# Kernel optimization log

Hardware: AMD Instinct MI355X
Metric: run time of the kernel (lower is better)

Reference implementation:

```python
import jax, jax.numpy as jnp
import numpy as np

VOCAB = 512
EMB = 256
HID = 64
T_HORIZON = 0.05


def setup_inputs() -> dict:
    key = jax.random.key(0)
    ks = jax.random.split(key, 6)
    B, L = 32, 4096
    x = jax.random.randint(ks[0], (B, L), 0, VOCAB, dtype=jnp.int64 if jax.config.jax_enable_x64 else jnp.int32)
    emb_table = jax.random.normal(ks[1], (VOCAB, EMB), dtype=jnp.float32)
    W1 = jax.random.normal(ks[2], (EMB, HID), dtype=jnp.float32) * (1.0 / np.sqrt(EMB))
    b1 = jnp.zeros((HID,), dtype=jnp.float32)
    W2 = jax.random.normal(ks[3], (HID, VOCAB), dtype=jnp.float32) * (1.0 / np.sqrt(HID))
    b2 = jnp.full((VOCAB,), 0.1, dtype=jnp.float32)  # torch: bias.data.fill_(0.1)
    return {"x": x, "emb_table": emb_table, "W1": W1, "b1": b1, "W2": W2, "b2": b2, "steps": 5}


def reference(x, emb_table, W1, b1, W2, b2, steps):
    """Vectorized Gillespie-style Markov jump simulation.

    Equivalent to the torch loop: intensity is computed once per step from the
    current state, then every (b, l) position samples a candidate next state
    from softmax(intensity) with the self-transition zeroed and renormalized
    (== categorical over logits with the current state masked to -inf), and
    accepts it with prob 1 - exp(-rate * dt).
    """
    V = emb_table.shape[0]
    dt = T_HORIZON / steps
    key = jax.random.key(42)
    keys = jax.random.split(key, steps)
    vocab_ids = jnp.arange(V)

    def step(x_t, k):
        # intensity: [B, L, V]
        h = jax.nn.relu(emb_table[x_t] @ W1 + b1)
        intensity = h @ W2 + b2
        # mask self-transition (softmax * (1 - onehot) then renormalize)
        self_mask = x_t[..., None] == vocab_ids  # [B, L, V] bool
        masked_logits = jnp.where(self_mask, -jnp.inf, intensity)
        k1, k2 = jax.random.split(k)
        next_state = jax.random.categorical(k1, masked_logits)  # [B, L]
        rate = jnp.take_along_axis(intensity, next_state[..., None], axis=-1)[..., 0]
        accept_prob = 1.0 - jnp.exp(-rate * dt)
        u = jax.random.uniform(k2, x_t.shape, dtype=rate.dtype)
        x_t = jnp.where(u < accept_prob, next_state.astype(x_t.dtype), x_t)
        return x_t, None

    x_final, _ = jax.lax.scan(step, x, keys)
    return x_final
```

## Files before the change

kernel.cpp:

```cpp
#include <hip/hip_runtime.h>
#include <stdint.h>


#define VOCAB 512
#define EMB   256
#define HID   64
#define NPOS  (32 * 4096)
#define STEPS 5
#define PPW   8
#define NWAVES (NPOS / PPW)

__host__ __device__ __forceinline__ void tf2x32(uint32_t k0, uint32_t k1,
                                                uint32_t x0, uint32_t x1,
                                                uint32_t& o0, uint32_t& o1) {
  uint32_t ks2 = k0 ^ k1 ^ 0x1BD11BDAu;
  x0 += k0; x1 += k1;
#define TFR(r) { x0 += x1; x1 = (x1 << (r)) | (x1 >> (32 - (r))); x1 ^= x0; }
  TFR(13) TFR(15) TFR(26) TFR(6)
  x0 += k1;  x1 += ks2 + 1u;
  TFR(17) TFR(29) TFR(16) TFR(24)
  x0 += ks2; x1 += k0 + 2u;
  TFR(13) TFR(15) TFR(26) TFR(6)
  x0 += k0;  x1 += k1 + 3u;
  TFR(17) TFR(29) TFR(16) TFR(24)
  x0 += k1;  x1 += ks2 + 4u;
  TFR(13) TFR(15) TFR(26) TFR(6)
  x0 += ks2; x1 += k0 + 5u;
#undef TFR
  o0 = x0; o1 = x1;
}

struct Keys {
  uint32_t k1a[STEPS], k1b[STEPS];
  uint32_t k2a[STEPS], k2b[STEPS];
};

__global__ __launch_bounds__(512)
void build_table(const float* __restrict__ emb,
                 const float* __restrict__ W1,
                 const float* __restrict__ b1,
                 const float* __restrict__ W2,
                 const float* __restrict__ b2,
                 float* __restrict__ I,
                 float* __restrict__ pthr) {
  const int s   = blockIdx.x;
  const int tid = threadIdx.x;
  __shared__ double part[8][HID];
  __shared__ double hd[HID];
  __shared__ float  redmax[8];

  const int hid = tid & (HID - 1);
  const int kq  = tid >> 6;
  const float* e = emb + s * EMB;
  double acc = 0.0;
#pragma unroll
  for (int k = kq; k < EMB; k += 8)
    acc += (double)e[k] * (double)W1[k * HID + hid];
  part[kq][hid] = acc;
  __syncthreads();
  if (kq == 0) {
    const double a = ((part[0][hid] + part[1][hid]) + (part[2][hid] + part[3][hid]))
                   + ((part[4][hid] + part[5][hid]) + (part[6][hid] + part[7][hid]));
    const float m = (float)a + b1[hid];
    hd[hid] = (double)(m > 0.0f ? m : 0.0f);
  }
  __syncthreads();

  double acc2 = 0.0;
#pragma unroll
  for (int k = 0; k < HID; ++k)
    acc2 += hd[k] * (double)W2[k * VOCAB + tid];
  const float val = (float)acc2 + b2[tid];
  I[s * VOCAB + tid] = val;

  float lmax = val;
  for (int off = 32; off > 0; off >>= 1)
    lmax = fmaxf(lmax, __shfl_xor(lmax, off, 64));
  if ((tid & 63) == 0) redmax[tid >> 6] = lmax;
  __syncthreads();
  if (tid == 0) {
    float m = redmax[0];
#pragma unroll
    for (int i = 1; i < 8; ++i) m = fmaxf(m, redmax[i]);
    const float z = (-m) * 0.01f;
    pthr[s] = 1.0f - (float)exp((double)z);
  }
}

__global__ __launch_bounds__(256)
void markov_kernel(const int* __restrict__ x_in,
                   const float* __restrict__ I,
                   const float* __restrict__ pthr,
                   int* __restrict__ x_out,
                   Keys K) {
  __shared__ float sp[VOCAB];
  sp[threadIdx.x]       = pthr[threadIdx.x];
  sp[threadIdx.x + 256] = pthr[threadIdx.x + 256];
  __syncthreads();

  const int gtid = blockIdx.x * blockDim.x + threadIdx.x;
  const int wave = gtid >> 6;
  const int lane = gtid & 63;
  const int base = wave * PPW;
  const float TINYF = 1.17549435e-38f;

  const int qp = lane / 5;
  const int qt = lane - qp * 5;
  float u40 = 0.0f;
  if (lane < PPW * STEPS) {
    uint32_t w0, w1;
    tf2x32(K.k2a[qt], K.k2b[qt], 0u, (uint32_t)(base + qp), w0, w1);
    u40 = __uint_as_float((((w0 ^ w1) >> 9) | 0x3f800000u)) - 1.0f;
  }
  int scur = (lane < PPW) ? x_in[base + lane] : 0;

  const int s_of_q = __shfl(scur, qp, 64);
  const bool cand = (lane < PPW * STEPS) && (u40 < sp[s_of_q]);
  unsigned long long mask = __ballot(cand);

  while (mask) {
    const int q = (int)__builtin_ctzll(mask);
    mask &= mask - 1;
    const int p = q / 5;
    const int t = q - p * 5;
    const int s = __builtin_amdgcn_readfirstlane(__shfl(scur, p, 64));

    const float* row = I + s * VOCAB;
    float best = -__builtin_inff();
    int bidx = 0;
    const uint32_t fbase = ((uint32_t)(base + p) << 9) + (uint32_t)lane;
#pragma unroll
    for (int j = 0; j < VOCAB / 64; ++j) {
      const int v = lane + (j << 6);
      uint32_t w0, w1;
      tf2x32(K.k1a[t], K.k1b[t], 0u, fbase + ((uint32_t)j << 6), w0, w1);
      const uint32_t bits = w0 ^ w1;
      float uf = __uint_as_float((bits >> 9) | 0x3f800000u) - 1.0f;
      if (uf == 0.0f) uf = TINYF;
      const float g = -logf(-logf(uf));
      if (v != s) {
        const float val = row[v] + g;
        if (val > best) { best = val; bidx = v; }
      }
    }
    for (int off = 32; off > 0; off >>= 1) {
      const float ob = __shfl_xor(best, off, 64);
      const int   oi = __shfl_xor(bidx, off, 64);
      if (ob > best || (ob == best && oi < bidx)) { best = ob; bidx = oi; }
    }
    bidx = __builtin_amdgcn_readfirstlane(bidx);
    const float rate = row[bidx];
    const float z = (-rate) * 0.01f;
    const float pacc = 1.0f - (float)exp((double)z);
    const float u = __shfl(u40, q, 64);
    if (u < pacc) {
      if (lane == p) scur = bidx;
      const unsigned long long fut =
          (((1ull << (p * 5 + 5)) - 1) & ~((1ull << (q + 1)) - 1));
      const float pnew = sp[bidx];
      const unsigned long long nb = __ballot(u40 < pnew) & fut;
      mask = (mask & ~fut) | nb;
    }
  }
  if (lane < PPW) x_out[base + lane] = scur;
}

extern "C" void kernel_launch(void* const* d_in, const int* in_sizes, int n_in,
                              void* d_out, int out_size, void* d_ws, size_t ws_size,
                              hipStream_t stream) {
  const int*   x   = (const int*)d_in[0];
  const float* emb = (const float*)d_in[1];
  const float* W1  = (const float*)d_in[2];
  const float* b1  = (const float*)d_in[3];
  const float* W2  = (const float*)d_in[4];
  const float* b2  = (const float*)d_in[5];
  float* I    = (float*)d_ws;
  float* pthr = (float*)d_ws + VOCAB * VOCAB;
  int* out = (int*)d_out;

  Keys K;
  for (int t = 0; t < STEPS; ++t) {
    uint32_t Sa, Sb;
    tf2x32(0u, 42u, 0u, (uint32_t)t, Sa, Sb);
    tf2x32(Sa, Sb, 0u, 0u, K.k1a[t], K.k1b[t]);
    tf2x32(Sa, Sb, 0u, 1u, K.k2a[t], K.k2b[t]);
  }

  build_table<<<VOCAB, 512, 0, stream>>>(emb, W1, b1, W2, b2, I, pthr);
  markov_kernel<<<(NWAVES * 64) / 256, 256, 0, stream>>>(x, I, pthr, out, K);
}
```

Measured before the change: 121.5 us.

## Drop shared threshold table, shrink blocks, hoist row loads ahead of RNG

The per-block shared-memory copy of the acceptance threshold table and its barrier are removed, and thresholds are now read directly from global memory. Blocks shrink to 128 threads with a min-blocks-per-CU launch bound. The 8 intensity-row loads are issued before the Threefry computations so their latency overlaps with the RNG ALU work. This trades barrier and LDS setup per block for scattered global reads and possible register pressure from the hoisted arrays.

After: 116.0 us. 4.5% less time.

```diff
diff --git a/kernel.cpp b/kernel.cpp
--- a/kernel.cpp
+++ b/kernel.cpp
@@ -2,13 +2,13 @@
 #include <stdint.h>
 
 
-#define VOCAB 512
-#define EMB   256
-#define HID   64
-#define NPOS  (32 * 4096)
-#define STEPS 5
-#define PPW   8
-#define NWAVES (NPOS / PPW)
+#define VOCAB  512
+#define EMB    256
+#define HID    64
+#define NPOS   (32 * 4096)
+#define STEPS  5
+#define PPW    8
+#define CHUNKS (NPOS / PPW)
 
 __host__ __device__ __forceinline__ void tf2x32(uint32_t k0, uint32_t k1,
                                                 uint32_t x0, uint32_t x1,
@@ -87,35 +87,30 @@
   }
 }
 
-__global__ __launch_bounds__(256)
+__global__ __launch_bounds__(128, 4)
 void markov_kernel(const int* __restrict__ x_in,
                    const float* __restrict__ I,
                    const float* __restrict__ pthr,
                    int* __restrict__ x_out,
                    Keys K) {
-  __shared__ float sp[VOCAB];
-  sp[threadIdx.x]       = pthr[threadIdx.x];
-  sp[threadIdx.x + 256] = pthr[threadIdx.x + 256];
-  __syncthreads();
-
-  const int gtid = blockIdx.x * blockDim.x + threadIdx.x;
-  const int wave = gtid >> 6;
-  const int lane = gtid & 63;
-  const int base = wave * PPW;
+  const int lane  = threadIdx.x & 63;
+  const int chunk = (blockIdx.x << 1) | (threadIdx.x >> 6);
+  const int base  = chunk * PPW;
+  const int qp = lane / 5;
+  const int qt = lane - qp * 5;
   const float TINYF = 1.17549435e-38f;
 
-  const int qp = lane / 5;
-  const int qt = lane - qp * 5;
+  int scur = (lane < PPW) ? x_in[base + lane] : 0;
+
   float u40 = 0.0f;
   if (lane < PPW * STEPS) {
     uint32_t w0, w1;
     tf2x32(K.k2a[qt], K.k2b[qt], 0u, (uint32_t)(base + qp), w0, w1);
     u40 = __uint_as_float((((w0 ^ w1) >> 9) | 0x3f800000u)) - 1.0f;
   }
-  int scur = (lane < PPW) ? x_in[base + lane] : 0;
 
   const int s_of_q = __shfl(scur, qp, 64);
-  const bool cand = (lane < PPW * STEPS) && (u40 < sp[s_of_q]);
+  const bool cand = (lane < PPW * STEPS) && (u40 < pthr[s_of_q]);
   unsigned long long mask = __ballot(cand);
 
   while (mask) {
@@ -126,20 +121,30 @@
     const int s = __builtin_amdgcn_readfirstlane(__shfl(scur, p, 64));
 
     const float* row = I + s * VOCAB;
+    float rv[8];
+#pragma unroll
+    for (int j = 0; j < 8; ++j)
+      rv[j] = row[lane + (j << 6)];
+
+    const uint32_t fbase = ((uint32_t)(base + p) << 9) + (uint32_t)lane;
+    uint32_t bits[8];
+#pragma unroll
+    for (int j = 0; j < 8; ++j) {
+      uint32_t w0, w1;
+      tf2x32(K.k1a[t], K.k1b[t], 0u, fbase + ((uint32_t)j << 6), w0, w1);
+      bits[j] = w0 ^ w1;
+    }
+
     float best = -__builtin_inff();
     int bidx = 0;
-    const uint32_t fbase = ((uint32_t)(base + p) << 9) + (uint32_t)lane;
 #pragma unroll
-    for (int j = 0; j < VOCAB / 64; ++j) {
+    for (int j = 0; j < 8; ++j) {
+      float ufv = __uint_as_float((bits[j] >> 9) | 0x3f800000u) - 1.0f;
+      if (ufv == 0.0f) ufv = TINYF;
+      const float g = -logf(-logf(ufv));
       const int v = lane + (j << 6);
-      uint32_t w0, w1;
-      tf2x32(K.k1a[t], K.k1b[t], 0u, fbase + ((uint32_t)j << 6), w0, w1);
-      const uint32_t bits = w0 ^ w1;
-      float uf = __uint_as_float((bits >> 9) | 0x3f800000u) - 1.0f;
-      if (uf == 0.0f) uf = TINYF;
-      const float g = -logf(-logf(uf));
       if (v != s) {
-        const float val = row[v] + g;
+        const float val = rv[j] + g;
         if (val > best) { best = val; bidx = v; }
       }
     }
@@ -157,7 +162,7 @@
       if (lane == p) scur = bidx;
       const unsigned long long fut =
           (((1ull << (p * 5 + 5)) - 1) & ~((1ull << (q + 1)) - 1));
-      const float pnew = sp[bidx];
+      const float pnew = pthr[bidx];
       const unsigned long long nb = __ballot(u40 < pnew) & fut;
       mask = (mask & ~fut) | nb;
     }
@@ -187,5 +192,5 @@
   }
 
   build_table<<<VOCAB, 512, 0, stream>>>(emb, W1, b1, W2, b2, I, pthr);
-  markov_kernel<<<(NWAVES * 64) / 256, 256, 0, stream>>>(x, I, pthr, out, K);
+  markov_kernel<<<CHUNKS / 2, 128, 0, stream>>>(x, I, pthr, out, K);
 }
```
